# Optimization experiments

Hardware: AMD Instinct MI355X
Metric: run time of the kernel (lower is better)

## Reference

```python
import jax, jax.numpy as jnp
import numpy as np

K, B, D, H, C, T = 3, 512, 1024, 512, 48, 25  # num_TAB, batch, linear_dim, hidden, n_classes, max_len

def setup_inputs() -> dict:
    key = jax.random.key(0)
    ks = jax.random.split(key, 18)
    rn = lambda k, s, sc=0.02: (jax.random.normal(k, s, jnp.float32) * sc)
    return {
        'S_ppps': jax.random.normal(ks[0], (K, B, D), jnp.float32),
        'R_ppps': jax.random.normal(ks[1], (K, B, D), jnp.float32),
        'cls_W': rn(ks[2], (K, 2 * D, C)), 'cls_b': jnp.zeros((K, C), jnp.float32),
        'dur_W': rn(ks[3], (K * D, 1)), 'dur_b': jnp.zeros((1,), jnp.float32),
        'lin_W': rn(ks[4], (2 * K * D + K * C, D + 1)), 'lin_b': jnp.zeros((D + 1,), jnp.float32),
        'W_ih': rn(ks[5], (4 * H, D + 1)), 'W_hh': rn(ks[6], (4 * H, H)),
        'b_ih': jnp.zeros((4 * H,), jnp.float32), 'b_hh': jnp.zeros((4 * H,), jnp.float32),
        'Wp': rn(ks[7], (H, C)), 'bp': jnp.zeros((C,), jnp.float32),
        'Wdur': rn(ks[8], (D + H, 1)), 'bdur': jnp.zeros((1,), jnp.float32),
        'embed': rn(ks[9], (C, D), 1.0),
        'Wattn': rn(ks[10], (H, D)),
    }

def reference(S_ppps, R_ppps, cls_W, cls_b, dur_W, dur_b, lin_W, lin_b,
              W_ih, W_hh, b_ih, b_hh, Wp, bp, Wdur, bdur, embed, Wattn):
    S_stack = jnp.transpose(S_ppps, (1, 0, 2))            # [B,K,D] (torch.stack(S_ppps,1))
    # per-TAB classifiers: Y[i] = softmax(Linear(cat(S_i,R_i)))
    SR = jnp.concatenate([S_ppps, R_ppps], axis=-1)       # [K,B,2D]
    Y = jax.nn.softmax(jnp.einsum('kbd,kdc->kbc', SR, cls_W) + cls_b[:, None, :], axis=-1)  # [K,B,C]
    Yf = jnp.transpose(Y, (1, 0, 2)).reshape(B, K * C)    # cat(Y0..Yk) feature-wise
    Sf = jnp.transpose(S_ppps, (1, 0, 2)).reshape(B, K * D)
    Rf = jnp.transpose(R_ppps, (1, 0, 2)).reshape(B, K * D)
    feat = jnp.concatenate([Yf, Sf, Rf], axis=1)          # [B, K*C + 2*K*D]
    x0 = feat @ lin_W + lin_b                             # [B, D+1]
    curr_dur = Rf @ dur_W + dur_b                         # [B,1]
    inv_sqrt_d = 1.0 / np.sqrt(D).astype(np.float32)

    def step(carry, _):
        x, h, c, prev_h = carry
        gates = x @ W_ih.T + b_ih + h @ W_hh.T + b_hh     # [B,4H], torch gate order i,f,g,o
        i_g, f_g, g_g, o_g = jnp.split(gates, 4, axis=1)
        c = jax.nn.sigmoid(f_g) * c + jax.nn.sigmoid(i_g) * jnp.tanh(g_g)
        h = jax.nn.sigmoid(o_g) * jnp.tanh(c)
        logits = h @ Wp + bp                              # [B,C]
        q = (h @ Wattn) * inv_sqrt_d                      # [B,D]
        aw = jax.nn.softmax(jnp.einsum('bd,bkd->bk', q, S_stack), axis=-1)
        att = jnp.einsum('bk,bkd->bd', aw, S_stack)       # [B,D]
        dur = jnp.concatenate([att, prev_h], axis=1) @ Wdur + bdur  # [B,1]
        labels = jnp.argmax(logits, axis=1)
        probs = jax.nn.softmax(logits, axis=1)
        nx = jnp.concatenate([embed[labels], dur], axis=1)  # [B,D+1]
        return (nx, h, c, h), (labels, probs, dur[:, 0], att)

    z = jnp.zeros((B, H), x0.dtype)
    _, (labels_t, probs_t, dur_t, att_t) = jax.lax.scan(step, (x0, z, z, z), None, length=T)
    curr_action = jnp.sum(Y, axis=0)                      # [B,C]
    pred_class_probs = jnp.transpose(probs_t, (1, 0, 2))  # [B,T,C]
    pred_action_durations = jnp.concatenate([curr_dur, dur_t.T], axis=1)  # [B,T+1]
    return (labels_t, pred_class_probs, curr_action, pred_action_durations, att_t)
```

## Files before the change

kernel.cpp:

```cpp
#include <hip/hip_runtime.h>
#include <math.h>

#define B 512
#define D 1024
#define H 512
#define C 48
#define K 3
#define T 25
#define DP1 1025
#define G4H 2048
#define NC 2112
#define NCV 2096
#define KP 1056
#define FK 6304

typedef _Float16 f16;
typedef _Float16 half8 __attribute__((ext_vector_type(8)));
typedef float floatx4 __attribute__((ext_vector_type(4)));

__device__ __forceinline__ float sigf(float x){ return 1.0f/(1.0f+__expf(-x)); }
__device__ __forceinline__ float tanhf_fast(float x){
    float t = __expf(-2.0f*fabsf(x));
    float r = (1.0f-t)/(1.0f+t);
    return x<0.f ? -r : r;
}

template<int NT, int MODE>
__global__ __launch_bounds__(256)
void k_gemm(const f16* __restrict__ Ahi, const f16* __restrict__ Alo,
            const f16* __restrict__ Bhi, const f16* __restrict__ Blo,
            float* __restrict__ Cc, const float* __restrict__ bias,
            int M, int Nvalid, int Ktot, int lda, int ldb, int ldc,
            int ksl, size_t cstride, int MB, int Z, int zmaj,
            const f16* __restrict__ Yh, const f16* __restrict__ Yl,
            const float* __restrict__ Sf, const float* __restrict__ Rf)
{
    __shared__ __align__(16) f16 Ash[2][64][40];
    __shared__ __align__(16) f16 Asl[2][64][40];
    __shared__ __align__(16) f16 Bsh[2][NT][40];
    __shared__ __align__(16) f16 Bsl[2][NT][40];
    int t = threadIdx.x;
    int mblk, nblk, z;
    if (zmaj){
        z = blockIdx.x % Z;
        int rest = blockIdx.x / Z;
        mblk = rest % MB; nblk = rest / MB;
    } else {
        int chunk = gridDim.x >> 3;
        int g = (blockIdx.x & 7)*chunk + (blockIdx.x >> 3);
        int mz = g % (MB*Z);
        nblk = g / (MB*Z);
        mblk = mz / Z;
        z    = mz % Z;
    }
    int m0 = mblk*64, n0 = nblk*NT;
    int kbase = z*ksl;
    int kcnt = (z==Z-1)? (Ktot-kbase) : ksl;
    int nIter = kcnt >> 5;
    int r = t>>2, seg = t&3;
    const bool ldB = (r < NT);
    half8 rah, ral, rbh, rbl;
    float4 fA0, fA1;

    auto LOAD = [&](int k0){
        int kk = k0 + seg*8;
        if (ldB){
            size_t off = (size_t)(n0+r)*ldb + kbase + kk;
            rbh = *(const half8*)(Bhi + off);
            rbl = *(const half8*)(Blo + off);
        }
        int m = m0 + r;
        if (MODE==0){
            if (m < M){
                size_t off = (size_t)m*lda + kbase + kk;
                rah = *(const half8*)(Ahi + off);
                ral = *(const half8*)(Alo + off);
            } else {
                #pragma unroll
                for (int i=0;i<8;i++){ rah[i]=(f16)0; ral[i]=(f16)0; }
            }
        } else {
            int kabs = kbase + kk;
            if (kabs < 144){
                rah = *(const half8*)(Yh + (size_t)m*144 + kabs);
                ral = *(const half8*)(Yl + (size_t)m*144 + kabs);
            } else if (kabs < 6288){
                int kp = kabs - 144;
                const float* src = (kp < 3*D)
                    ? (Sf + (size_t)(kp>>10)*(B*D) + (size_t)m*D + (kp&(D-1)))
                    : (Rf + (size_t)((kp-3*D)>>10)*(B*D) + (size_t)m*D + ((kp-3*D)&(D-1)));
                fA0 = *(const float4*)src;
                fA1 = *(const float4*)(src+4);
            } else {
                #pragma unroll
                for (int i=0;i<8;i++){ rah[i]=(f16)0; ral[i]=(f16)0; }
            }
        }
    };
    auto CONV = [&](int k0){
        int kk = k0 + seg*8;
        int kabs = kbase + kk;
        if (kabs >= 144 && kabs < 6288){
            float fv[8]={fA0.x,fA0.y,fA0.z,fA0.w,fA1.x,fA1.y,fA1.z,fA1.w};
            #pragma unroll
            for (int i=0;i<8;i++){
                f16 h=(f16)fv[i];
                rah[i]=h; ral[i]=(f16)(fv[i]-(float)h);
            }
        }
    };

    LOAD(0);
    if (MODE==1) CONV(0);
    int lane = t&63, wv = t>>6;
    int lrow = lane&15, quad = lane>>4;
    floatx4 acc[NT/16] = {};
    int cur = 0;
    for (int it=0; it<nIter; ++it){
        *(half8*)&Ash[cur][r][seg*8] = rah;
        *(half8*)&Asl[cur][r][seg*8] = ral;
        if (ldB){
            *(half8*)&Bsh[cur][r][seg*8] = rbh;
            *(half8*)&Bsl[cur][r][seg*8] = rbl;
        }
        if (it+1 < nIter) LOAD((it+1)<<5);
        asm volatile("s_waitcnt lgkmcnt(0)" ::: "memory");
        __builtin_amdgcn_s_barrier();
        half8 ah = *(const half8*)&Ash[cur][wv*16+lrow][quad*8];
        half8 al = *(const half8*)&Asl[cur][wv*16+lrow][quad*8];
        #pragma unroll
        for (int j=0;j<NT/16;j++){
            half8 bh = *(const half8*)&Bsh[cur][j*16+lrow][quad*8];
            half8 bl = *(const half8*)&Bsl[cur][j*16+lrow][quad*8];
            acc[j] = __builtin_amdgcn_mfma_f32_16x16x32_f16(ah, bh, acc[j], 0,0,0);
            acc[j] = __builtin_amdgcn_mfma_f32_16x16x32_f16(al, bh, acc[j], 0,0,0);
            acc[j] = __builtin_amdgcn_mfma_f32_16x16x32_f16(ah, bl, acc[j], 0,0,0);
        }
        if (MODE==1 && it+1 < nIter) CONV((it+1)<<5);
        cur ^= 1;
    }
    float* Cz = Cc + (size_t)z*cstride;
    #pragma unroll
    for (int j=0;j<NT/16;j++){
        int col = n0 + j*16 + lrow;
        if (col >= Nvalid) continue;
        float bv = bias ? bias[col] : 0.f;
        #pragma unroll
        for (int i=0;i<4;i++){
            int row = m0 + wv*16 + quad*4 + i;
            if (row < M) Cz[(size_t)row*ldc + col] = acc[j][i] + bv;
        }
    }
}


__global__ void k_bt_build(const float* __restrict__ src, f16* __restrict__ hi, f16* __restrict__ lo,
                           int Ksrc, int Nsrc, int ld_src, int NB, int KB, float scale){
    __shared__ float tile[32][33];
    int k0 = blockIdx.x*32, n0 = blockIdx.y*32;
    int lx = threadIdx.x & 31, ly = threadIdx.x >> 5;
    for (int rr=0; rr<32; rr+=8){
        int k2 = k0+ly+rr, n = n0+lx;
        tile[ly+rr][lx] = (k2<Ksrc && n<Nsrc)? src[(size_t)k2*ld_src+n]*scale : 0.f;
    }
    __syncthreads();
    for (int rr=0; rr<32; rr+=8){
        int n = n0+ly+rr, k2 = k0+lx;
        if (n<NB && k2<KB){
            float v = tile[lx][ly+rr];
            f16 h=(f16)v;
            hi[(size_t)n*KB+k2]=h;
            lo[(size_t)n*KB+k2]=(f16)(v-(float)h);
        }
    }
}

__global__ void k_permrows(const float* __restrict__ src, f16* __restrict__ hi, f16* __restrict__ lo,
                           int src_ld, int dst_ld, int kvalid){
    int idx = blockIdx.x*256+threadIdx.x;
    if (idx >= G4H*dst_ld) return;
    int p = idx/dst_ld, k2 = idx%dst_ld;
    int j = p>>2, g = p&3, gi = (g<<9)|j;
    float v = (k2<kvalid)? src[(size_t)gi*src_ld + k2] : 0.f;
    f16 h=(f16)v;
    hi[idx]=h; lo[idx]=(f16)(v-(float)h);
}

__global__ void k_cvt(const float* __restrict__ src, f16* __restrict__ hi, f16* __restrict__ lo,
                      int M, int ld_src, int nvalid, int ld_dst, float scale){
    int idx = blockIdx.x*256+threadIdx.x;
    if (idx >= M*ld_dst) return;
    int m = idx/ld_dst, n = idx%ld_dst;
    float v = (n<nvalid)? src[(size_t)m*ld_src+n]*scale : 0.f;
    f16 h=(f16)v; hi[idx]=h; lo[idx]=(f16)(v-(float)h);
}

__global__ void k_cvtY(const float* __restrict__ Y, f16* __restrict__ hi, f16* __restrict__ lo){
    int idx = blockIdx.x*256+threadIdx.x;
    if (idx >= B*144) return;
    int b = idx/144, k2 = idx%144;
    float v = Y[((size_t)(k2/C)*B + b)*C + (k2%C)];
    f16 h=(f16)v; hi[idx]=h; lo[idx]=(f16)(v-(float)h);
}

__global__ void k_zeroh(f16* a, f16* b2, int n){
    int i = blockIdx.x*256+threadIdx.x; if (i<n){ a[i]=(f16)0; b2[i]=(f16)0; }
}

__global__ void k_prep(const float* __restrict__ bih, const float* __restrict__ bhh,
                       const float* __restrict__ bp, const float* __restrict__ Wih,
                       float* __restrict__ bias2p, float* __restrict__ biascat,
                       float* __restrict__ wl){
    int i = blockIdx.x*256 + threadIdx.x;
    if (i < G4H){
        int g=i&3, j=i>>2; int gi=(g<<9)|j;
        bias2p[i]=bih[gi]+bhh[gi];
        wl[i]=Wih[(size_t)gi*DP1 + 1024];
    }
    if (i < C) biascat[i]=bp[i];
}

__global__ void k_cls(const float* __restrict__ S, const float* __restrict__ R,
                      const float* __restrict__ clsW, const float* __restrict__ clsb,
                      float* __restrict__ Y){
    int kb = blockIdx.x; int k = kb / B; int b = kb % B;
    int t = threadIdx.x;
    __shared__ float sr[64];
    __shared__ float lg[C];
    __shared__ float mred[2];
    float acc = (t<C) ? clsb[k*C+t] : 0.f;
    const float* W = clsW + (size_t)k*2*D*C;
    for (int i0=0; i0<2*D; i0+=64){
        int i = i0 + t;
        sr[t] = (i < D) ? S[((size_t)k*B+b)*D + i] : R[((size_t)k*B+b)*D + (i-D)];
        __syncthreads();
        if (t < C){ for (int ii=0; ii<64; ++ii) acc += sr[ii]*W[(size_t)(i0+ii)*C + t]; }
        __syncthreads();
    }
    if (t<C) lg[t]=acc;
    __syncthreads();
    if (t==0){
        float m=lg[0]; for(int c2=1;c2<C;c2++) m=fmaxf(m,lg[c2]);
        float s=0.f; for(int c2=0;c2<C;c2++) s+=expf(lg[c2]-m);
        mred[0]=m; mred[1]=s;
    }
    __syncthreads();
    if (t<C) Y[((size_t)k*B+b)*C + t] = expf(lg[t]-mred[0])/mred[1];
}

__global__ void k_curr_action(const float* __restrict__ Y, float* __restrict__ outca){
    int i = blockIdx.x*256+threadIdx.x; if (i>=B*C) return;
    int b=i/C, c2=i%C;
    outca[i] = Y[((size_t)0*B+b)*C+c2] + Y[((size_t)1*B+b)*C+c2] + Y[((size_t)2*B+b)*C+c2];
}

__global__ void k_dur0(const float* __restrict__ R, const float* __restrict__ durW,
                       const float* __restrict__ durb, float* __restrict__ outpad){
    int b = blockIdx.x; int t = threadIdx.x;
    __shared__ float red[256];
    float p=0.f;
    for (int i=t; i<K*D; i+=256){ int k=i>>10, d=i&1023; p += R[((size_t)k*B+b)*D+d]*durW[i]; }
    red[t]=p; __syncthreads();
    for (int s=128;s>0;s>>=1){ if(t<s) red[t]+=red[t+s]; __syncthreads(); }
    if (t==0) outpad[(size_t)b*(T+1)] = red[0] + durb[0];
}

__global__ void k_red(float* __restrict__ dst, const float* __restrict__ src, int parts, size_t pstride,
                      int M, int Nld, int Nvalid, const float* __restrict__ bias){
    int idx = blockIdx.x*256+threadIdx.x;
    if (idx >= M*Nld) return;
    int n = idx % Nld;
    float v = 0.f;
    if (n < Nvalid){
        for (int p=0;p<parts;p++) v += src[(size_t)p*pstride + idx];
        if (bias) v += bias[n];
    }
    dst[idx]=v;
}

__global__ void k_redcvt(const float* __restrict__ src, int parts, size_t pstride,
                         const float* __restrict__ bias, f16* __restrict__ hi, f16* __restrict__ lo){
    int idx = blockIdx.x*256+threadIdx.x;
    if (idx >= 512*KP) return;
    int m = idx/KP, n = idx%KP;
    float v = 0.f;
    if (n < DP1){
        for (int p=0;p<parts;p++) v += src[(size_t)p*pstride + (size_t)m*1028 + n];
        v += bias[n];
    }
    f16 h=(f16)v; hi[idx]=h; lo[idx]=(f16)(v-(float)h);
}


__global__ void k_lstm0(const float* __restrict__ gxp, int parts, size_t pstride,
                        const float* __restrict__ bias2p,
                        float* __restrict__ c, f16* __restrict__ hhi, f16* __restrict__ hlo){
    int idx = blockIdx.x*256+threadIdx.x; if (idx>=B*H) return;
    int r=idx>>9, j=idx&511;
    float4 g = *(const float4*)&gxp[(size_t)r*G4H + (j<<2)];
    if (parts==2){
        float4 g2 = *(const float4*)&gxp[pstride + (size_t)r*G4H + (j<<2)];
        g.x+=g2.x; g.y+=g2.y; g.z+=g2.z; g.w+=g2.w;
    }
    float4 bb = *(const float4*)&bias2p[j<<2];
    g.x+=bb.x; g.y+=bb.y; g.z+=bb.z; g.w+=bb.w;
    float cn = sigf(g.x)*tanhf_fast(g.z);
    c[idx]=cn;
    float hv = sigf(g.w)*tanhf_fast(cn);
    f16 h=(f16)hv; hhi[idx]=h; hlo[idx]=(f16)(hv-(float)h);
}

template<int PARTS>
__global__ void k_postapply(const float* __restrict__ rawg, size_t pstride,
                       const float* __restrict__ S, const float* __restrict__ V,
                       const f16* __restrict__ hchi, const f16* __restrict__ hclo,
                       const f16* __restrict__ holdhi, const f16* __restrict__ holdlo,
                       const float* __restrict__ E, const float* __restrict__ wl,
                       const float* __restrict__ biascat,
                       const float* __restrict__ Wdur, const float* __restrict__ bdur,
                       float* __restrict__ outlab, float* __restrict__ outprobs,
                       float* __restrict__ outatt, float* __restrict__ outpad,
                       float* __restrict__ c, f16* __restrict__ hNhi, f16* __restrict__ hNlo,
                       int tstep, int doLstm)
{
    int b=blockIdx.x, t=threadIdx.x;
    int lane=t&63, wv=t>>6;
    __shared__ float aw[3];
    __shared__ float redw[4][8];
    __shared__ int sbest;
    __shared__ float sdv;
    const float* z0 = rawg + (size_t)b*NC;
    if (t<64){
        float lgv = -3.0e38f;
        if (t<C){
            float v = 0.f;
            #pragma unroll
            for (int p=0;p<PARTS;p++) v += z0[(size_t)p*pstride + G4H + t];
            lgv = v + biascat[t];
        }
        float m = lgv; int bi = t;
        #pragma unroll
        for (int s2=32;s2>0;s2>>=1){
            float om=__shfl_xor(m,s2); int ob=__shfl_xor(bi,s2);
            if (om>m || (om==m && ob<bi)){ m=om; bi=ob; }
        }
        float e=(t<C)? __expf(lgv-m):0.f;
        float ss=e;
        #pragma unroll
        for (int s2=32;s2>0;s2>>=1) ss+=__shfl_xor(ss,s2);
        if (t<C) outprobs[(size_t)b*(T*C)+tstep*C+t]=e/ss;
        if (t==0){
            sbest=bi;
            outlab[(size_t)tstep*B+b]=(float)bi;
        }
    }
    float hv_t = (float)hchi[(size_t)b*H + t] + (float)hclo[(size_t)b*H + t];
    float p0 = hv_t * V[((size_t)(0*B+b))*H + t];
    float p1 = hv_t * V[((size_t)(1*B+b))*H + t];
    float p2 = hv_t * V[((size_t)(2*B+b))*H + t];
    #pragma unroll
    for (int s2=32;s2>0;s2>>=1){
        p0 += __shfl_xor(p0,s2); p1 += __shfl_xor(p1,s2); p2 += __shfl_xor(p2,s2);
    }
    if (lane==0){ redw[0][wv]=p0; redw[1][wv]=p1; redw[2][wv]=p2; }
    __syncthreads();
    if (t==0){
        float a0=0.f,a1=0.f,a2=0.f;
        #pragma unroll
        for (int w=0;w<8;w++){ a0+=redw[0][w]; a1+=redw[1][w]; a2+=redw[2][w]; }
        float m=fmaxf(a0,fmaxf(a1,a2));
        float e0=__expf(a0-m), e1=__expf(a1-m), e2=__expf(a2-m);
        float si=1.f/(e0+e1+e2);
        aw[0]=e0*si; aw[1]=e1*si; aw[2]=e2*si;
    }
    __syncthreads();
    float a0=aw[0],a1=aw[1],a2=aw[2];
    const float* S0  = S + (size_t)b*D;
    const float* S1  = S0 + (size_t)B*D;
    const float* S2p = S1 + (size_t)B*D;
    float dp = 0.f;
    float* attp = outatt + (size_t)tstep*B*D + (size_t)b*D;
    {
        int d = t<<1;
        float2 s0 = *(const float2*)(S0+d);
        float2 s1 = *(const float2*)(S1+d);
        float2 s2 = *(const float2*)(S2p+d);
        float2 w2 = *(const float2*)(Wdur+d);
        float2 av;
        av.x = a0*s0.x+a1*s1.x+a2*s2.x;
        av.y = a0*s0.y+a1*s1.y+a2*s2.y;
        *(float2*)(attp+d) = av;
        dp += av.x*w2.x+av.y*w2.y;
    }
    if (holdhi){
        float hvo = (float)holdhi[(size_t)b*H+t] + (float)holdlo[(size_t)b*H+t];
        dp += hvo * Wdur[D+t];
    }
    #pragma unroll
    for (int s2=32;s2>0;s2>>=1) dp += __shfl_xor(dp,s2);
    if (lane==0) redw[3][wv]=dp;
    __syncthreads();
    if (t==0){
        float dv=0.f;
        #pragma unroll
        for (int w=0;w<8;w++) dv+=redw[3][w];
        dv += bdur[0];
        outpad[(size_t)b*(T+1)+tstep+1]=dv; sdv=dv;
    }
    __syncthreads();
    if (doLstm){
        int lb=sbest; float dv=sdv;
        int j=t;
        float4 g4 = *(const float4*)&z0[4*j];
        #pragma unroll
        for (int p=1;p<PARTS;p++){
            float4 h4 = *(const float4*)&z0[(size_t)p*pstride + 4*j];
            g4.x+=h4.x; g4.y+=h4.y; g4.z+=h4.z; g4.w+=h4.w;
        }
        float4 e4 = *(const float4*)&E[(size_t)lb*G4H+4*j];
        float4 w4 = *(const float4*)&wl[4*j];
        float gi = g4.x+e4.x+dv*w4.x;
        float gf = g4.y+e4.y+dv*w4.y;
        float gg = g4.z+e4.z+dv*w4.z;
        float go = g4.w+e4.w+dv*w4.w;
        size_t ci=(size_t)b*H+j;
        float cn = sigf(gf)*c[ci] + sigf(gi)*tanhf_fast(gg);
        c[ci]=cn;
        float hv = sigf(go)*tanhf_fast(cn);
        f16 hh=(f16)hv;
        hNhi[ci]=hh; hNlo[ci]=(f16)(hv-(float)hh);
    }
}


extern "C" void kernel_launch(void* const* d_in, const int* in_sizes, int n_in,
                              void* d_out, int out_size, void* d_ws, size_t ws_size,
                              hipStream_t stream) {
    const float* S    = (const float*)d_in[0];
    const float* R    = (const float*)d_in[1];
    const float* clsW = (const float*)d_in[2];
    const float* clsb = (const float*)d_in[3];
    const float* durW = (const float*)d_in[4];
    const float* durb = (const float*)d_in[5];
    const float* linW = (const float*)d_in[6];
    const float* linb = (const float*)d_in[7];
    const float* Wih  = (const float*)d_in[8];
    const float* Whh  = (const float*)d_in[9];
    const float* bih  = (const float*)d_in[10];
    const float* bhh  = (const float*)d_in[11];
    const float* Wp   = (const float*)d_in[12];
    const float* bp   = (const float*)d_in[13];
    const float* Wdur = (const float*)d_in[14];
    const float* bdur = (const float*)d_in[15];
    const float* embed= (const float*)d_in[16];
    const float* Wattn= (const float*)d_in[17];

    float* out = (float*)d_out;
    float* outlab   = out;
    float* outprobs = out + 12800;
    float* outca    = out + 627200;
    float* outpad   = out + 651776;
    float* outatt   = out + 665088;

    float* ws = (float*)d_ws;
    float* E       = ws + 0;
    float* wl      = ws + 98304;
    float* bias2p  = ws + 100352;
    float* biascat = ws + 102400;
    float* c       = ws + 102464;
    f16*   hAhi    = (f16*)(ws + 364608);
    f16*   hAlo    = (f16*)(ws + 495680);
    f16*   hBhi    = (f16*)(ws + 626752);
    f16*   hBlo    = (f16*)(ws + 757824);
    f16*   Yhi     = (f16*)(ws + 889920);
    f16*   Ylo     = (f16*)(ws + 926784);
    float* Y       = ws + 963648;
    f16*   watthi  = (f16*)(ws + 1037376);
    f16*   wattlo  = (f16*)(ws + 1299520);
    f16*   x0hi    = (f16*)(ws + 1563712);
    f16*   x0lo    = (f16*)(ws + 1834048);
    f16*   embhi   = (f16*)(ws + 2104384);
    f16*   emblo   = (f16*)(ws + 2129728);
    const size_t SB = 2155072;
    f16*   lwthi   = (f16*)(ws + SB);
    f16*   lwtlo   = (f16*)(ws + SB + 3429376);
    float* x0part  = ws + SB + 6858752;
    f16*   Wcthi   = (f16*)(ws + SB);
    f16*   Wctlo   = (f16*)(ws + SB + 540672);
    f16*   Shi     = (f16*)(ws + SB + 1081344);
    f16*   Slo     = (f16*)(ws + SB + 1867776);
    float* Vbuf    = ws + SB + 2654208;
    f16*   Wihphi  = (f16*)(ws + SB + 3440640);
    f16*   Wihplo  = (f16*)(ws + SB + 4521984);
    float* rawg    = ws + SB + 3440640;
    float* gpart   = ws + SB + 5603328;

    int ZX0, ksl_x0;
    if      (ws_size >= (size_t)52898048){ ZX0=8; ksl_x0=800;  }
    else if (ws_size >= (size_t)44476672){ ZX0=4; ksl_x0=1600; }
    else                                 { ZX0=2; ksl_x0=3168; }
    const int ZGX = 2, ksl_gx = 544;
    const int ZE  = 4, ksl_e  = 256;

    k_prep<<<8,256,0,stream>>>(bih,bhh,bp,Wih,bias2p,biascat,wl);
    k_cls<<<K*B,64,0,stream>>>(S,R,clsW,clsb,Y);
    k_curr_action<<<(B*C+255)/256,256,0,stream>>>(Y,outca);
    k_cvtY<<<(B*144+255)/256,256,0,stream>>>(Y,Yhi,Ylo);
    k_dur0<<<B,256,0,stream>>>(R,durW,durb,outpad);
    k_bt_build<<<dim3((FK+31)/32,(1088+31)/32),256,0,stream>>>(linW,lwthi,lwtlo,6288,1025,1025,1088,FK,1.f);
    k_gemm<32,1><<<8*33*ZX0,256,0,stream>>>(nullptr,nullptr,lwthi,lwtlo,x0part,nullptr,
                                            512,1028,FK,0,FK,1028,ksl_x0,(size_t)512*1028,8,ZX0,1,
                                            Yhi,Ylo,S,R);
    k_redcvt<<<(512*KP+255)/256,256,0,stream>>>(x0part,ZX0,(size_t)512*1028,linb,x0hi,x0lo);
    k_permrows<<<(G4H*KP+255)/256,256,0,stream>>>(Wih,Wihphi,Wihplo,DP1,KP,DP1);
    k_gemm<64,0><<<8*32*ZGX,256,0,stream>>>(x0hi,x0lo,Wihphi,Wihplo,gpart,nullptr,
                                            512,G4H,KP,KP,KP,G4H,ksl_gx,(size_t)512*G4H,8,ZGX,0,
                                            nullptr,nullptr,nullptr,nullptr);
    k_lstm0<<<(B*H+255)/256,256,0,stream>>>(gpart,ZGX,(size_t)512*G4H,bias2p,c,hAhi,hAlo);
    k_cvt<<<(48*KP+255)/256,256,0,stream>>>(embed,embhi,emblo,48,1024,1024,KP,1.f);
    k_gemm<64,0><<<1*32*ZE,256,0,stream>>>(embhi,emblo,Wihphi,Wihplo,gpart,nullptr,
                                           48,G4H,KP,KP,KP,G4H,ksl_e,(size_t)48*G4H,1,ZE,0,
                                           nullptr,nullptr,nullptr,nullptr);
    k_red<<<(48*G4H+255)/256,256,0,stream>>>(E,gpart,ZE,(size_t)48*G4H,48,G4H,G4H,bias2p);
    k_cvt<<<(1536*1024+255)/256,256,0,stream>>>(S,Shi,Slo,1536,1024,1024,1024,1.f);
    k_cvt<<<(512*1024+255)/256,256,0,stream>>>(Wattn,watthi,wattlo,512,1024,1024,1024,0.03125f);
    k_gemm<64,0><<<24*8,256,0,stream>>>(Shi,Slo,watthi,wattlo,Vbuf,nullptr,
                                        1536,512,1024,1024,1024,512,1024,0,24,1,0,
                                        nullptr,nullptr,nullptr,nullptr);
    k_permrows<<<(G4H*512+255)/256,256,0,stream>>>(Whh,Wcthi,Wctlo,H,H,H);
    k_bt_build<<<dim3(16,2),256,0,stream>>>(Wp,Wcthi+(size_t)2048*512,Wctlo+(size_t)2048*512,
                                            512,48,48,48,512,1.f);
    k_zeroh<<<32,256,0,stream>>>(Wcthi+(size_t)2096*512,Wctlo+(size_t)2096*512,16*512);

    size_t pstr = (size_t)512*NC;
    f16 *hCurHi=hAhi, *hCurLo=hAlo, *hPrvHi=hBhi, *hPrvLo=hBlo;
    for (int t=0;t<T;t++){
        k_gemm<32,0><<<8*66,256,0,stream>>>(hCurHi,hCurLo,Wcthi,Wctlo,rawg,nullptr,
                                            512,NCV,H,H,H,NC,512,pstr,8,1,0,
                                            nullptr,nullptr,nullptr,nullptr);
        k_postapply<1><<<B,512,0,stream>>>(rawg,pstr,S,Vbuf,hCurHi,hCurLo,
                                        (t==0)?nullptr:hPrvHi,(t==0)?nullptr:hPrvLo,
                                        E,wl,biascat,Wdur,bdur,
                                        outlab,outprobs,outatt,outpad,
                                        c,hPrvHi,hPrvLo,t,(t<T-1)?1:0);
        f16* th=hPrvHi; hPrvHi=hCurHi; hCurHi=th;
        f16* tl=hPrvLo; hPrvLo=hCurLo; hCurLo=tl;
    }
}
```

Baseline: 859.3 us.

## Split-K recurrent GEMM and collapse post-step kernel to one wavefront per row

```diff
diff --git a/kernel.cpp b/kernel.cpp
--- a/kernel.cpp
+++ b/kernel.cpp
@@ -311,124 +311,126 @@
 }
 
 template<int PARTS>
-__global__ void k_postapply(const float* __restrict__ rawg, size_t pstride,
-                       const float* __restrict__ S, const float* __restrict__ V,
-                       const f16* __restrict__ hchi, const f16* __restrict__ hclo,
-                       const f16* __restrict__ holdhi, const f16* __restrict__ holdlo,
-                       const float* __restrict__ E, const float* __restrict__ wl,
-                       const float* __restrict__ biascat,
-                       const float* __restrict__ Wdur, const float* __restrict__ bdur,
-                       float* __restrict__ outlab, float* __restrict__ outprobs,
-                       float* __restrict__ outatt, float* __restrict__ outpad,
-                       float* __restrict__ c, f16* __restrict__ hNhi, f16* __restrict__ hNlo,
-                       int tstep, int doLstm)
+__global__ __launch_bounds__(64)
+void k_postwave(const float* __restrict__ rawg, size_t pstride,
+                const float* __restrict__ S, const float* __restrict__ V,
+                const f16* __restrict__ hchi, const f16* __restrict__ hclo,
+                const f16* __restrict__ holdhi, const f16* __restrict__ holdlo,
+                const float* __restrict__ E, const float* __restrict__ wl,
+                const float* __restrict__ biascat,
+                const float* __restrict__ Wdur, const float* __restrict__ bdur,
+                float* __restrict__ outlab, float* __restrict__ outprobs,
+                float* __restrict__ outatt, float* __restrict__ outpad,
+                float* __restrict__ c, f16* __restrict__ hNhi, f16* __restrict__ hNlo,
+                int tstep, int doLstm)
 {
-    int b=blockIdx.x, t=threadIdx.x;
-    int lane=t&63, wv=t>>6;
-    __shared__ float aw[3];
-    __shared__ float redw[4][8];
-    __shared__ int sbest;
-    __shared__ float sdv;
+    const int b = blockIdx.x, lane = threadIdx.x;
     const float* z0 = rawg + (size_t)b*NC;
-    if (t<64){
-        float lgv = -3.0e38f;
-        if (t<C){
-            float v = 0.f;
-            #pragma unroll
-            for (int p=0;p<PARTS;p++) v += z0[(size_t)p*pstride + G4H + t];
-            lgv = v + biascat[t];
-        }
-        float m = lgv; int bi = t;
+
+    float hv8[8], va0[8], va1[8], va2[8];
+    {
+        half8 hh = *(const half8*)(hchi + (size_t)b*H + lane*8);
+        half8 hl = *(const half8*)(hclo + (size_t)b*H + lane*8);
         #pragma unroll
-        for (int s2=32;s2>0;s2>>=1){
-            float om=__shfl_xor(m,s2); int ob=__shfl_xor(bi,s2);
-            if (om>m || (om==m && ob<bi)){ m=om; bi=ob; }
-        }
-        float e=(t<C)? __expf(lgv-m):0.f;
-        float ss=e;
+        for (int i=0;i<8;i++) hv8[i] = (float)hh[i] + (float)hl[i];
+        const float* V0 = V + ((size_t)(0*B+b))*H + lane*8;
+        const float* V1 = V + ((size_t)(1*B+b))*H + lane*8;
+        const float* V2 = V + ((size_t)(2*B+b))*H + lane*8;
+        *(float4*)va0 = *(const float4*)V0; *(float4*)(va0+4) = *(const float4*)(V0+4);
+        *(float4*)va1 = *(const float4*)V1; *(float4*)(va1+4) = *(const float4*)(V1+4);
+        *(float4*)va2 = *(const float4*)V2; *(float4*)(va2+4) = *(const float4*)(V2+4);
+    }
+
+    float lgv = -3.0e38f;
+    if (lane < C){
+        float v = 0.f;
         #pragma unroll
-        for (int s2=32;s2>0;s2>>=1) ss+=__shfl_xor(ss,s2);
-        if (t<C) outprobs[(size_t)b*(T*C)+tstep*C+t]=e/ss;
-        if (t==0){
-            sbest=bi;
-            outlab[(size_t)tstep*B+b]=(float)bi;
-        }
-    }
-    float hv_t = (float)hchi[(size_t)b*H + t] + (float)hclo[(size_t)b*H + t];
-    float p0 = hv_t * V[((size_t)(0*B+b))*H + t];
-    float p1 = hv_t * V[((size_t)(1*B+b))*H + t];
-    float p2 = hv_t * V[((size_t)(2*B+b))*H + t];
+        for (int p=0;p<PARTS;p++) v += z0[(size_t)p*pstride + G4H + lane];
+        lgv = v + biascat[lane];
+    }
+    float m = lgv; int bi = lane;
+    #pragma unroll
+    for (int s2=32;s2>0;s2>>=1){
+        float om = __shfl_xor(m, s2); int ob = __shfl_xor(bi, s2);
+        if (om>m || (om==m && ob<bi)){ m=om; bi=ob; }
+    }
+    float e = (lane<C)? __expf(lgv-m) : 0.f;
+    float ss = e;
+    #pragma unroll
+    for (int s2=32;s2>0;s2>>=1) ss += __shfl_xor(ss, s2);
+    if (lane<C) outprobs[(size_t)b*(T*C)+tstep*C+lane] = e/ss;
+    if (lane==0) outlab[(size_t)tstep*B+b] = (float)bi;
+
+    float p0=0.f,p1=0.f,p2=0.f;
+    #pragma unroll
+    for (int i=0;i<8;i++){ p0 += hv8[i]*va0[i]; p1 += hv8[i]*va1[i]; p2 += hv8[i]*va2[i]; }
     #pragma unroll
     for (int s2=32;s2>0;s2>>=1){
         p0 += __shfl_xor(p0,s2); p1 += __shfl_xor(p1,s2); p2 += __shfl_xor(p2,s2);
     }
-    if (lane==0){ redw[0][wv]=p0; redw[1][wv]=p1; redw[2][wv]=p2; }
-    __syncthreads();
-    if (t==0){
-        float a0=0.f,a1=0.f,a2=0.f;
-        #pragma unroll
-        for (int w=0;w<8;w++){ a0+=redw[0][w]; a1+=redw[1][w]; a2+=redw[2][w]; }
-        float m=fmaxf(a0,fmaxf(a1,a2));
-        float e0=__expf(a0-m), e1=__expf(a1-m), e2=__expf(a2-m);
-        float si=1.f/(e0+e1+e2);
-        aw[0]=e0*si; aw[1]=e1*si; aw[2]=e2*si;
-    }
-    __syncthreads();
-    float a0=aw[0],a1=aw[1],a2=aw[2];
+    float m3 = fmaxf(p0,fmaxf(p1,p2));
+    float e0 = __expf(p0-m3), e1 = __expf(p1-m3), e2 = __expf(p2-m3);
+    float si = 1.f/(e0+e1+e2);
+    float a0=e0*si, a1=e1*si, a2=e2*si;
+
     const float* S0  = S + (size_t)b*D;
     const float* S1  = S0 + (size_t)B*D;
     const float* S2p = S1 + (size_t)B*D;
+    float* attp = outatt + (size_t)tstep*B*D + (size_t)b*D;
     float dp = 0.f;
-    float* attp = outatt + (size_t)tstep*B*D + (size_t)b*D;
-    {
-        int d = t<<1;
-        float2 s0 = *(const float2*)(S0+d);
-        float2 s1 = *(const float2*)(S1+d);
-        float2 s2 = *(const float2*)(S2p+d);
-        float2 w2 = *(const float2*)(Wdur+d);
-        float2 av;
+    #pragma unroll
+    for (int i=0;i<4;i++){
+        int d = (lane + (i<<6))<<2;
+        float4 s0 = *(const float4*)(S0+d);
+        float4 s1 = *(const float4*)(S1+d);
+        float4 s2 = *(const float4*)(S2p+d);
+        float4 w4 = *(const float4*)(Wdur+d);
+        float4 av;
         av.x = a0*s0.x+a1*s1.x+a2*s2.x;
         av.y = a0*s0.y+a1*s1.y+a2*s2.y;
-        *(float2*)(attp+d) = av;
-        dp += av.x*w2.x+av.y*w2.y;
+        av.z = a0*s0.z+a1*s1.z+a2*s2.z;
+        av.w = a0*s0.w+a1*s1.w+a2*s2.w;
+        *(float4*)(attp+d) = av;
+        dp += av.x*w4.x+av.y*w4.y+av.z*w4.z+av.w*w4.w;
     }
     if (holdhi){
-        float hvo = (float)holdhi[(size_t)b*H+t] + (float)holdlo[(size_t)b*H+t];
-        dp += hvo * Wdur[D+t];
+        half8 oh = *(const half8*)(holdhi + (size_t)b*H + lane*8);
+        half8 ol = *(const half8*)(holdlo + (size_t)b*H + lane*8);
+        const float* wd = Wdur + D + lane*8;
+        float w8[8];
+        *(float4*)w8 = *(const float4*)wd; *(float4*)(w8+4) = *(const float4*)(wd+4);
+        #pragma unroll
+        for (int i=0;i<8;i++) dp += ((float)oh[i]+(float)ol[i]) * w8[i];
     }
     #pragma unroll
     for (int s2=32;s2>0;s2>>=1) dp += __shfl_xor(dp,s2);
-    if (lane==0) redw[3][wv]=dp;
-    __syncthreads();
-    if (t==0){
-        float dv=0.f;
+    float dv = dp + bdur[0];
+    if (lane==0) outpad[(size_t)b*(T+1)+tstep+1] = dv;
+
+    if (doLstm){
+        const float* Erow = E + (size_t)bi*G4H;
         #pragma unroll
-        for (int w=0;w<8;w++) dv+=redw[3][w];
-        dv += bdur[0];
-        outpad[(size_t)b*(T+1)+tstep+1]=dv; sdv=dv;
-    }
-    __syncthreads();
-    if (doLstm){
-        int lb=sbest; float dv=sdv;
-        int j=t;
-        float4 g4 = *(const float4*)&z0[4*j];
-        #pragma unroll
-        for (int p=1;p<PARTS;p++){
-            float4 h4 = *(const float4*)&z0[(size_t)p*pstride + 4*j];
-            g4.x+=h4.x; g4.y+=h4.y; g4.z+=h4.z; g4.w+=h4.w;
-        }
-        float4 e4 = *(const float4*)&E[(size_t)lb*G4H+4*j];
-        float4 w4 = *(const float4*)&wl[4*j];
-        float gi = g4.x+e4.x+dv*w4.x;
-        float gf = g4.y+e4.y+dv*w4.y;
-        float gg = g4.z+e4.z+dv*w4.z;
-        float go = g4.w+e4.w+dv*w4.w;
-        size_t ci=(size_t)b*H+j;
-        float cn = sigf(gf)*c[ci] + sigf(gi)*tanhf_fast(gg);
-        c[ci]=cn;
-        float hv = sigf(go)*tanhf_fast(cn);
-        f16 hh=(f16)hv;
-        hNhi[ci]=hh; hNlo[ci]=(f16)(hv-(float)hh);
+        for (int i=0;i<8;i++){
+            int j = lane + (i<<6);
+            float4 g4 = *(const float4*)(z0 + 4*j);
+            #pragma unroll
+            for (int p=1;p<PARTS;p++){
+                float4 h4 = *(const float4*)(z0 + (size_t)p*pstride + 4*j);
+                g4.x+=h4.x; g4.y+=h4.y; g4.z+=h4.z; g4.w+=h4.w;
+            }
+            float4 e4 = *(const float4*)(Erow + 4*j);
+            float4 w4 = *(const float4*)(wl + 4*j);
+            float gi = g4.x+e4.x+dv*w4.x;
+            float gf = g4.y+e4.y+dv*w4.y;
+            float gg = g4.z+e4.z+dv*w4.z;
+            float go = g4.w+e4.w+dv*w4.w;
+            size_t ci = (size_t)b*H+j;
+            float cn = sigf(gf)*c[ci] + sigf(gi)*tanhf_fast(gg);
+            c[ci] = cn;
+            float hv = sigf(go)*tanhf_fast(cn);
+            f16 hh = (f16)hv;
+            hNhi[ci]=hh; hNlo[ci]=(f16)(hv-(float)hh);
+        }
     }
 }
 
@@ -501,6 +503,7 @@
     else                                 { ZX0=2; ksl_x0=3168; }
     const int ZGX = 2, ksl_gx = 544;
     const int ZE  = 4, ksl_e  = 256;
+    const int ZSC = 2, ksl_sc = 256;
 
     k_prep<<<8,256,0,stream>>>(bih,bhh,bp,Wih,bias2p,biascat,wl);
     k_cls<<<K*B,64,0,stream>>>(S,R,clsW,clsb,Y);
@@ -535,14 +538,14 @@
     size_t pstr = (size_t)512*NC;
     f16 *hCurHi=hAhi, *hCurLo=hAlo, *hPrvHi=hBhi, *hPrvLo=hBlo;
     for (int t=0;t<T;t++){
-        k_gemm<32,0><<<8*66,256,0,stream>>>(hCurHi,hCurLo,Wcthi,Wctlo,rawg,nullptr,
-                                            512,NCV,H,H,H,NC,512,pstr,8,1,0,
-                                            nullptr,nullptr,nullptr,nullptr);
-        k_postapply<1><<<B,512,0,stream>>>(rawg,pstr,S,Vbuf,hCurHi,hCurLo,
-                                        (t==0)?nullptr:hPrvHi,(t==0)?nullptr:hPrvLo,
-                                        E,wl,biascat,Wdur,bdur,
-                                        outlab,outprobs,outatt,outpad,
-                                        c,hPrvHi,hPrvLo,t,(t<T-1)?1:0);
+        k_gemm<32,0><<<8*66*ZSC,256,0,stream>>>(hCurHi,hCurLo,Wcthi,Wctlo,rawg,nullptr,
+                                                512,NCV,H,H,H,NC,ksl_sc,pstr,8,ZSC,0,
+                                                nullptr,nullptr,nullptr,nullptr);
+        k_postwave<2><<<B,64,0,stream>>>(rawg,pstr,S,Vbuf,hCurHi,hCurLo,
+                                         (t==0)?nullptr:hPrvHi,(t==0)?nullptr:hPrvLo,
+                                         E,wl,biascat,Wdur,bdur,
+                                         outlab,outprobs,outatt,outpad,
+                                         c,hPrvHi,hPrvLo,t,(t<T-1)?1:0);
         f16* th=hPrvHi; hPrvHi=hCurHi; hCurHi=th;
         f16* tl=hPrvLo; hPrvLo=hCurLo; hCurLo=tl;
     }
```

Measured after the change: 917.3 us. +6.8%, slower.

## Pre-convert S/R to split-f16, split x0 GEMM in two, split-K recurrent GEMM

Applied to the files above, without the earlier changes.

```diff
diff --git a/kernel.cpp b/kernel.cpp
--- a/kernel.cpp
+++ b/kernel.cpp
@@ -12,7 +12,6 @@
 #define NC 2112
 #define NCV 2096
 #define KP 1056
-#define FK 6304
 
 typedef _Float16 f16;
 typedef _Float16 half8 __attribute__((ext_vector_type(8)));
@@ -31,28 +30,22 @@
             const f16* __restrict__ Bhi, const f16* __restrict__ Blo,
             float* __restrict__ Cc, const float* __restrict__ bias,
             int M, int Nvalid, int Ktot, int lda, int ldb, int ldc,
-            int ksl, size_t cstride, int MB, int Z, int zmaj,
+            int ksl, size_t cstride, int MB, int Z, int accu,
             const f16* __restrict__ Yh, const f16* __restrict__ Yl,
-            const float* __restrict__ Sf, const float* __restrict__ Rf)
+            const f16* __restrict__ Xh, const f16* __restrict__ Xl,
+            int kyoff, int kval)
 {
     __shared__ __align__(16) f16 Ash[2][64][40];
     __shared__ __align__(16) f16 Asl[2][64][40];
     __shared__ __align__(16) f16 Bsh[2][NT][40];
     __shared__ __align__(16) f16 Bsl[2][NT][40];
     int t = threadIdx.x;
-    int mblk, nblk, z;
-    if (zmaj){
-        z = blockIdx.x % Z;
-        int rest = blockIdx.x / Z;
-        mblk = rest % MB; nblk = rest / MB;
-    } else {
-        int chunk = gridDim.x >> 3;
-        int g = (blockIdx.x & 7)*chunk + (blockIdx.x >> 3);
-        int mz = g % (MB*Z);
-        nblk = g / (MB*Z);
-        mblk = mz / Z;
-        z    = mz % Z;
-    }
+    int chunk = gridDim.x >> 3;
+    int g = (blockIdx.x & 7)*chunk + (blockIdx.x >> 3);
+    int mz = g % (MB*Z);
+    int nblk = g / (MB*Z);
+    int mblk = mz / Z;
+    int z    = mz % Z;
     int m0 = mblk*64, n0 = nblk*NT;
     int kbase = z*ksl;
     int kcnt = (z==Z-1)? (Ktot-kbase) : ksl;
@@ -60,7 +53,6 @@
     int r = t>>2, seg = t&3;
     const bool ldB = (r < NT);
     half8 rah, ral, rbh, rbl;
-    float4 fA0, fA1;
 
     auto LOAD = [&](int k0){
         int kk = k0 + seg*8;
@@ -81,37 +73,22 @@
             }
         } else {
             int kabs = kbase + kk;
-            if (kabs < 144){
+            if (kabs < kyoff){
                 rah = *(const half8*)(Yh + (size_t)m*144 + kabs);
                 ral = *(const half8*)(Yl + (size_t)m*144 + kabs);
-            } else if (kabs < 6288){
-                int kp = kabs - 144;
-                const float* src = (kp < 3*D)
-                    ? (Sf + (size_t)(kp>>10)*(B*D) + (size_t)m*D + (kp&(D-1)))
-                    : (Rf + (size_t)((kp-3*D)>>10)*(B*D) + (size_t)m*D + ((kp-3*D)&(D-1)));
-                fA0 = *(const float4*)src;
-                fA1 = *(const float4*)(src+4);
+            } else if (kabs < kval){
+                int kp = kabs - kyoff;
+                size_t off = (size_t)(kp>>10)*((size_t)B*D) + (size_t)m*D + (kp&(D-1));
+                rah = *(const half8*)(Xh + off);
+                ral = *(const half8*)(Xl + off);
             } else {
                 #pragma unroll
                 for (int i=0;i<8;i++){ rah[i]=(f16)0; ral[i]=(f16)0; }
             }
         }
     };
-    auto CONV = [&](int k0){
-        int kk = k0 + seg*8;
-        int kabs = kbase + kk;
-        if (kabs >= 144 && kabs < 6288){
-            float fv[8]={fA0.x,fA0.y,fA0.z,fA0.w,fA1.x,fA1.y,fA1.z,fA1.w};
-            #pragma unroll
-            for (int i=0;i<8;i++){
-                f16 h=(f16)fv[i];
-                rah[i]=h; ral[i]=(f16)(fv[i]-(float)h);
-            }
-        }
-    };
 
     LOAD(0);
-    if (MODE==1) CONV(0);
     int lane = t&63, wv = t>>6;
     int lrow = lane&15, quad = lane>>4;
     floatx4 acc[NT/16] = {};
@@ -136,7 +113,6 @@
             acc[j] = __builtin_amdgcn_mfma_f32_16x16x32_f16(al, bh, acc[j], 0,0,0);
             acc[j] = __builtin_amdgcn_mfma_f32_16x16x32_f16(ah, bl, acc[j], 0,0,0);
         }
-        if (MODE==1 && it+1 < nIter) CONV((it+1)<<5);
         cur ^= 1;
     }
     float* Cz = Cc + (size_t)z*cstride;
@@ -148,7 +124,11 @@
         #pragma unroll
         for (int i=0;i<4;i++){
             int row = m0 + wv*16 + quad*4 + i;
-            if (row < M) Cz[(size_t)row*ldc + col] = acc[j][i] + bv;
+            if (row < M){
+                size_t idx = (size_t)row*ldc + col;
+                if (accu) Cz[idx] += acc[j][i];
+                else      Cz[idx]  = acc[j][i] + bv;
+            }
         }
     }
 }
@@ -482,51 +462,61 @@
     f16*   embhi   = (f16*)(ws + 2104384);
     f16*   emblo   = (f16*)(ws + 2129728);
     const size_t SB = 2155072;
-    f16*   lwthi   = (f16*)(ws + SB);
-    f16*   lwtlo   = (f16*)(ws + SB + 3429376);
-    float* x0part  = ws + SB + 6858752;
-    f16*   Wcthi   = (f16*)(ws + SB);
-    f16*   Wctlo   = (f16*)(ws + SB + 540672);
-    f16*   Shi     = (f16*)(ws + SB + 1081344);
-    f16*   Slo     = (f16*)(ws + SB + 1867776);
-    float* Vbuf    = ws + SB + 2654208;
-    f16*   Wihphi  = (f16*)(ws + SB + 3440640);
-    f16*   Wihplo  = (f16*)(ws + SB + 4521984);
-    float* rawg    = ws + SB + 3440640;
-    float* gpart   = ws + SB + 5603328;
-
-    int ZX0, ksl_x0;
-    if      (ws_size >= (size_t)52898048){ ZX0=8; ksl_x0=800;  }
-    else if (ws_size >= (size_t)44476672){ ZX0=4; ksl_x0=1600; }
-    else                                 { ZX0=2; ksl_x0=3168; }
+
+    f16*   Shi     = (f16*)(ws + SB);
+    f16*   Slo     = (f16*)(ws + SB + 786432);
+    const size_t SB2 = SB + 1572864;
+
+    f16*   lwtRh   = (f16*)(ws + SB2);
+    f16*   lwtRl   = (f16*)(ws + SB2 + 1671168);
+    f16*   lwtSYh  = (f16*)(ws + SB2);
+    f16*   lwtSYl  = (f16*)(ws + SB2 + 1758208);
+    f16*   Rhi     = (f16*)(ws + 7244352);
+    f16*   Rlo     = (f16*)(ws + 8030784);
+    float* x0part  = ws + 8817216;
+    f16*   Wcthi   = (f16*)(ws + SB2);
+    f16*   Wctlo   = (f16*)(ws + SB2 + 540672);
+    f16*   Wihphi  = (f16*)(ws + 4809280);
+    f16*   Wihplo  = (f16*)(ws + 5890624);
+    float* Vbuf    = ws + 6971968;
+    float* rawg    = ws + 7758400;
+    float* gpart   = ws + 7758400;
+
     const int ZGX = 2, ksl_gx = 544;
     const int ZE  = 4, ksl_e  = 256;
+    const int ZSC = 2, ksl_sc = 256;
 
     k_prep<<<8,256,0,stream>>>(bih,bhh,bp,Wih,bias2p,biascat,wl);
     k_cls<<<K*B,64,0,stream>>>(S,R,clsW,clsb,Y);
     k_curr_action<<<(B*C+255)/256,256,0,stream>>>(Y,outca);
     k_cvtY<<<(B*144+255)/256,256,0,stream>>>(Y,Yhi,Ylo);
     k_dur0<<<B,256,0,stream>>>(R,durW,durb,outpad);
-    k_bt_build<<<dim3((FK+31)/32,(1088+31)/32),256,0,stream>>>(linW,lwthi,lwtlo,6288,1025,1025,1088,FK,1.f);
-    k_gemm<32,1><<<8*33*ZX0,256,0,stream>>>(nullptr,nullptr,lwthi,lwtlo,x0part,nullptr,
-                                            512,1028,FK,0,FK,1028,ksl_x0,(size_t)512*1028,8,ZX0,1,
-                                            Yhi,Ylo,S,R);
-    k_redcvt<<<(512*KP+255)/256,256,0,stream>>>(x0part,ZX0,(size_t)512*1028,linb,x0hi,x0lo);
+    k_cvt<<<(1536*1024+255)/256,256,0,stream>>>(S,Shi,Slo,1536,1024,1024,1024,1.f);
+    k_cvt<<<(1536*1024+255)/256,256,0,stream>>>(R,Rhi,Rlo,1536,1024,1024,1024,1.f);
+    k_bt_build<<<dim3(96,34),256,0,stream>>>(linW+(size_t)3216*DP1,lwtRh,lwtRl,
+                                             3072,DP1,DP1,1088,3072,1.f);
+    k_gemm<32,1><<<8*33*2,256,0,stream>>>(nullptr,nullptr,lwtRh,lwtRl,x0part,nullptr,
+                                          512,1028,3072,0,3072,1028,1536,(size_t)512*1028,8,2,0,
+                                          nullptr,nullptr,Rhi,Rlo,0,3072);
+    k_bt_build<<<dim3(101,34),256,0,stream>>>(linW,lwtSYh,lwtSYl,3216,DP1,DP1,1088,3232,1.f);
+    k_gemm<32,1><<<8*33*2,256,0,stream>>>(nullptr,nullptr,lwtSYh,lwtSYl,x0part,nullptr,
+                                          512,1028,3232,0,3232,1028,1600,(size_t)512*1028,8,2,1,
+                                          Yhi,Ylo,Shi,Slo,144,3216);
+    k_redcvt<<<(512*KP+255)/256,256,0,stream>>>(x0part,2,(size_t)512*1028,linb,x0hi,x0lo);
     k_permrows<<<(G4H*KP+255)/256,256,0,stream>>>(Wih,Wihphi,Wihplo,DP1,KP,DP1);
     k_gemm<64,0><<<8*32*ZGX,256,0,stream>>>(x0hi,x0lo,Wihphi,Wihplo,gpart,nullptr,
                                             512,G4H,KP,KP,KP,G4H,ksl_gx,(size_t)512*G4H,8,ZGX,0,
-                                            nullptr,nullptr,nullptr,nullptr);
+                                            nullptr,nullptr,nullptr,nullptr,0,0);
     k_lstm0<<<(B*H+255)/256,256,0,stream>>>(gpart,ZGX,(size_t)512*G4H,bias2p,c,hAhi,hAlo);
     k_cvt<<<(48*KP+255)/256,256,0,stream>>>(embed,embhi,emblo,48,1024,1024,KP,1.f);
     k_gemm<64,0><<<1*32*ZE,256,0,stream>>>(embhi,emblo,Wihphi,Wihplo,gpart,nullptr,
                                            48,G4H,KP,KP,KP,G4H,ksl_e,(size_t)48*G4H,1,ZE,0,
-                                           nullptr,nullptr,nullptr,nullptr);
+                                           nullptr,nullptr,nullptr,nullptr,0,0);
     k_red<<<(48*G4H+255)/256,256,0,stream>>>(E,gpart,ZE,(size_t)48*G4H,48,G4H,G4H,bias2p);
-    k_cvt<<<(1536*1024+255)/256,256,0,stream>>>(S,Shi,Slo,1536,1024,1024,1024,1.f);
     k_cvt<<<(512*1024+255)/256,256,0,stream>>>(Wattn,watthi,wattlo,512,1024,1024,1024,0.03125f);
     k_gemm<64,0><<<24*8,256,0,stream>>>(Shi,Slo,watthi,wattlo,Vbuf,nullptr,
                                         1536,512,1024,1024,1024,512,1024,0,24,1,0,
-                                        nullptr,nullptr,nullptr,nullptr);
+                                        nullptr,nullptr,nullptr,nullptr,0,0);
     k_permrows<<<(G4H*512+255)/256,256,0,stream>>>(Whh,Wcthi,Wctlo,H,H,H);
     k_bt_build<<<dim3(16,2),256,0,stream>>>(Wp,Wcthi+(size_t)2048*512,Wctlo+(size_t)2048*512,
                                             512,48,48,48,512,1.f);
@@ -535,10 +525,10 @@
     size_t pstr = (size_t)512*NC;
     f16 *hCurHi=hAhi, *hCurLo=hAlo, *hPrvHi=hBhi, *hPrvLo=hBlo;
     for (int t=0;t<T;t++){
-        k_gemm<32,0><<<8*66,256,0,stream>>>(hCurHi,hCurLo,Wcthi,Wctlo,rawg,nullptr,
-                                            512,NCV,H,H,H,NC,512,pstr,8,1,0,
-                                            nullptr,nullptr,nullptr,nullptr);
-        k_postapply<1><<<B,512,0,stream>>>(rawg,pstr,S,Vbuf,hCurHi,hCurLo,
+        k_gemm<32,0><<<8*66*ZSC,256,0,stream>>>(hCurHi,hCurLo,Wcthi,Wctlo,rawg,nullptr,
+                                                512,NCV,H,H,H,NC,ksl_sc,pstr,8,ZSC,0,
+                                                nullptr,nullptr,nullptr,nullptr,0,0);
+        k_postapply<2><<<B,512,0,stream>>>(rawg,pstr,S,Vbuf,hCurHi,hCurLo,
                                         (t==0)?nullptr:hPrvHi,(t==0)?nullptr:hPrvLo,
                                         E,wl,biascat,Wdur,bdur,
                                         outlab,outprobs,outatt,outpad,
```

Measured after the change: 884.2 us. +2.9%, slower.

## Move per-TAB classifier onto split-fp16 MFMA GEMM and split-K the recurrent GEMM

Applied to the files above, without the earlier changes.

```diff
diff --git a/kernel.cpp b/kernel.cpp
--- a/kernel.cpp
+++ b/kernel.cpp
@@ -28,10 +28,10 @@
 template<int NT, int MODE>
 __global__ __launch_bounds__(256)
 void k_gemm(const f16* __restrict__ Ahi, const f16* __restrict__ Alo,
-            const f16* __restrict__ Bhi, const f16* __restrict__ Blo,
+            const f16* __restrict__ Bhi_, const f16* __restrict__ Blo_,
             float* __restrict__ Cc, const float* __restrict__ bias,
             int M, int Nvalid, int Ktot, int lda, int ldb, int ldc,
-            int ksl, size_t cstride, int MB, int Z, int zmaj,
+            int ksl, size_t cstride, int MB, int Z, int zmaj, int msel, size_t bsel,
             const f16* __restrict__ Yh, const f16* __restrict__ Yl,
             const float* __restrict__ Sf, const float* __restrict__ Rf)
 {
@@ -53,6 +53,9 @@
         mblk = mz / Z;
         z    = mz % Z;
     }
+    const f16* Bhi = Bhi_;
+    const f16* Blo = Blo_;
+    if (msel){ size_t so = (size_t)(mblk/msel)*bsel; Bhi += so; Blo += so; }
     int m0 = mblk*64, n0 = nblk*NT;
     int kbase = z*ksl;
     int kcnt = (z==Z-1)? (Ktot-kbase) : ksl;
@@ -195,6 +198,36 @@
     f16 h=(f16)v; hi[idx]=h; lo[idx]=(f16)(v-(float)h);
 }
 
+__global__ void k_cvtSR(const float* __restrict__ S, const float* __restrict__ R,
+                        f16* __restrict__ hi, f16* __restrict__ lo){
+    int idx = blockIdx.x*256+threadIdx.x;
+    if (idx >= 1536*2048) return;
+    int m = idx>>11, kk = idx&2047;
+    float v = (kk<1024)? S[((size_t)m<<10)+kk] : R[((size_t)m<<10)+kk-1024];
+    f16 h=(f16)v; hi[idx]=h; lo[idx]=(f16)(v-(float)h);
+}
+
+__global__ __launch_bounds__(64)
+void k_clssm(const float* __restrict__ part, const float* __restrict__ clsb,
+             float* __restrict__ Y){
+    int row = blockIdx.x, lane = threadIdx.x;
+    float v = -3.0e38f;
+    if (lane < C){
+        float s = 0.f;
+        #pragma unroll
+        for (int z=0;z<4;z++) s += part[(size_t)z*(1536*64) + (size_t)row*64 + lane];
+        v = s + clsb[(row>>9)*C + lane];
+    }
+    float m = v;
+    #pragma unroll
+    for (int s2=32;s2>0;s2>>=1) m = fmaxf(m, __shfl_xor(m,s2));
+    float e = (lane<C)? expf(v-m) : 0.f;
+    float ss = e;
+    #pragma unroll
+    for (int s2=32;s2>0;s2>>=1) ss += __shfl_xor(ss,s2);
+    if (lane<C) Y[(size_t)row*C + lane] = e/ss;
+}
+
 __global__ void k_cvtY(const float* __restrict__ Y, f16* __restrict__ hi, f16* __restrict__ lo){
     int idx = blockIdx.x*256+threadIdx.x;
     if (idx >= B*144) return;
@@ -218,34 +251,6 @@
         wl[i]=Wih[(size_t)gi*DP1 + 1024];
     }
     if (i < C) biascat[i]=bp[i];
-}
-
-__global__ void k_cls(const float* __restrict__ S, const float* __restrict__ R,
-                      const float* __restrict__ clsW, const float* __restrict__ clsb,
-                      float* __restrict__ Y){
-    int kb = blockIdx.x; int k = kb / B; int b = kb % B;
-    int t = threadIdx.x;
-    __shared__ float sr[64];
-    __shared__ float lg[C];
-    __shared__ float mred[2];
-    float acc = (t<C) ? clsb[k*C+t] : 0.f;
-    const float* W = clsW + (size_t)k*2*D*C;
-    for (int i0=0; i0<2*D; i0+=64){
-        int i = i0 + t;
-        sr[t] = (i < D) ? S[((size_t)k*B+b)*D + i] : R[((size_t)k*B+b)*D + (i-D)];
-        __syncthreads();
-        if (t < C){ for (int ii=0; ii<64; ++ii) acc += sr[ii]*W[(size_t)(i0+ii)*C + t]; }
-        __syncthreads();
-    }
-    if (t<C) lg[t]=acc;
-    __syncthreads();
-    if (t==0){
-        float m=lg[0]; for(int c2=1;c2<C;c2++) m=fmaxf(m,lg[c2]);
-        float s=0.f; for(int c2=0;c2<C;c2++) s+=expf(lg[c2]-m);
-        mred[0]=m; mred[1]=s;
-    }
-    __syncthreads();
-    if (t<C) Y[((size_t)k*B+b)*C + t] = expf(lg[t]-mred[0])/mred[1];
 }
 
 __global__ void k_curr_action(const float* __restrict__ Y, float* __restrict__ outca){
@@ -482,9 +487,17 @@
     f16*   embhi   = (f16*)(ws + 2104384);
     f16*   emblo   = (f16*)(ws + 2129728);
     const size_t SB = 2155072;
+
+    f16*   srch    = (f16*)(ws + SB);
+    f16*   srcl    = (f16*)(ws + SB + 1572864);
+    f16*   cwth    = (f16*)(ws + SB + 3145728);
+    f16*   cwtl    = (f16*)(ws + SB + 3342336);
+    float* clspart = ws + SB + 3538944;
+
     f16*   lwthi   = (f16*)(ws + SB);
     f16*   lwtlo   = (f16*)(ws + SB + 3429376);
     float* x0part  = ws + SB + 6858752;
+
     f16*   Wcthi   = (f16*)(ws + SB);
     f16*   Wctlo   = (f16*)(ws + SB + 540672);
     f16*   Shi     = (f16*)(ws + SB + 1081344);
@@ -501,31 +514,43 @@
     else                                 { ZX0=2; ksl_x0=3168; }
     const int ZGX = 2, ksl_gx = 544;
     const int ZE  = 4, ksl_e  = 256;
+    const int ZSC = 2, ksl_sc = 256;
 
     k_prep<<<8,256,0,stream>>>(bih,bhh,bp,Wih,bias2p,biascat,wl);
-    k_cls<<<K*B,64,0,stream>>>(S,R,clsW,clsb,Y);
+    k_cvtSR<<<(1536*2048+255)/256,256,0,stream>>>(S,R,srch,srcl);
+    for (int k=0;k<K;k++)
+        k_bt_build<<<dim3(64,2),256,0,stream>>>(clsW+(size_t)k*2048*C,
+                                                cwth+(size_t)k*64*2048, cwtl+(size_t)k*64*2048,
+                                                2048,C,C,64,2048,1.f);
+    k_gemm<32,0><<<24*4*2,256,0,stream>>>(srch,srcl,cwth,cwtl,clspart,nullptr,
+                                          1536,C,2048,2048,2048,64,512,(size_t)1536*64,24,4,0,
+                                          8,(size_t)64*2048,
+                                          nullptr,nullptr,nullptr,nullptr);
+    k_clssm<<<1536,64,0,stream>>>(clspart,clsb,Y);
     k_curr_action<<<(B*C+255)/256,256,0,stream>>>(Y,outca);
     k_cvtY<<<(B*144+255)/256,256,0,stream>>>(Y,Yhi,Ylo);
     k_dur0<<<B,256,0,stream>>>(R,durW,durb,outpad);
+
     k_bt_build<<<dim3((FK+31)/32,(1088+31)/32),256,0,stream>>>(linW,lwthi,lwtlo,6288,1025,1025,1088,FK,1.f);
     k_gemm<32,1><<<8*33*ZX0,256,0,stream>>>(nullptr,nullptr,lwthi,lwtlo,x0part,nullptr,
-                                            512,1028,FK,0,FK,1028,ksl_x0,(size_t)512*1028,8,ZX0,1,
+                                            512,1028,FK,0,FK,1028,ksl_x0,(size_t)512*1028,8,ZX0,1,0,0,
                                             Yhi,Ylo,S,R);
     k_redcvt<<<(512*KP+255)/256,256,0,stream>>>(x0part,ZX0,(size_t)512*1028,linb,x0hi,x0lo);
+
     k_permrows<<<(G4H*KP+255)/256,256,0,stream>>>(Wih,Wihphi,Wihplo,DP1,KP,DP1);
     k_gemm<64,0><<<8*32*ZGX,256,0,stream>>>(x0hi,x0lo,Wihphi,Wihplo,gpart,nullptr,
-                                            512,G4H,KP,KP,KP,G4H,ksl_gx,(size_t)512*G4H,8,ZGX,0,
+                                            512,G4H,KP,KP,KP,G4H,ksl_gx,(size_t)512*G4H,8,ZGX,0,0,0,
                                             nullptr,nullptr,nullptr,nullptr);
     k_lstm0<<<(B*H+255)/256,256,0,stream>>>(gpart,ZGX,(size_t)512*G4H,bias2p,c,hAhi,hAlo);
     k_cvt<<<(48*KP+255)/256,256,0,stream>>>(embed,embhi,emblo,48,1024,1024,KP,1.f);
     k_gemm<64,0><<<1*32*ZE,256,0,stream>>>(embhi,emblo,Wihphi,Wihplo,gpart,nullptr,
-                                           48,G4H,KP,KP,KP,G4H,ksl_e,(size_t)48*G4H,1,ZE,0,
+                                           48,G4H,KP,KP,KP,G4H,ksl_e,(size_t)48*G4H,1,ZE,0,0,0,
                                            nullptr,nullptr,nullptr,nullptr);
     k_red<<<(48*G4H+255)/256,256,0,stream>>>(E,gpart,ZE,(size_t)48*G4H,48,G4H,G4H,bias2p);
     k_cvt<<<(1536*1024+255)/256,256,0,stream>>>(S,Shi,Slo,1536,1024,1024,1024,1.f);
     k_cvt<<<(512*1024+255)/256,256,0,stream>>>(Wattn,watthi,wattlo,512,1024,1024,1024,0.03125f);
     k_gemm<64,0><<<24*8,256,0,stream>>>(Shi,Slo,watthi,wattlo,Vbuf,nullptr,
-                                        1536,512,1024,1024,1024,512,1024,0,24,1,0,
+                                        1536,512,1024,1024,1024,512,1024,0,24,1,0,0,0,
                                         nullptr,nullptr,nullptr,nullptr);
     k_permrows<<<(G4H*512+255)/256,256,0,stream>>>(Whh,Wcthi,Wctlo,H,H,H);
     k_bt_build<<<dim3(16,2),256,0,stream>>>(Wp,Wcthi+(size_t)2048*512,Wctlo+(size_t)2048*512,
@@ -535,10 +560,10 @@
     size_t pstr = (size_t)512*NC;
     f16 *hCurHi=hAhi, *hCurLo=hAlo, *hPrvHi=hBhi, *hPrvLo=hBlo;
     for (int t=0;t<T;t++){
-        k_gemm<32,0><<<8*66,256,0,stream>>>(hCurHi,hCurLo,Wcthi,Wctlo,rawg,nullptr,
-                                            512,NCV,H,H,H,NC,512,pstr,8,1,0,
-                                            nullptr,nullptr,nullptr,nullptr);
-        k_postapply<1><<<B,512,0,stream>>>(rawg,pstr,S,Vbuf,hCurHi,hCurLo,
+        k_gemm<32,0><<<8*66*ZSC,256,0,stream>>>(hCurHi,hCurLo,Wcthi,Wctlo,rawg,nullptr,
+                                                512,NCV,H,H,H,NC,ksl_sc,pstr,8,ZSC,0,0,0,
+                                                nullptr,nullptr,nullptr,nullptr);
+        k_postapply<2><<<B,512,0,stream>>>(rawg,pstr,S,Vbuf,hCurHi,hCurLo,
                                         (t==0)?nullptr:hPrvHi,(t==0)?nullptr:hPrvLo,
                                         E,wl,biascat,Wdur,bdur,
                                         outlab,outprobs,outatt,outpad,
```

Result: no change. 847.9 us (-1.3%).
